# Kernel tuning notes

Hardware: AMD Instinct MI355X
Metric: run time of the kernel (lower is better)

## Reference

```python
import jax, jax.numpy as jnp
import numpy as np

HEADS = 8
DIM_HEAD = 64
SCALE = 10.0
EPS = 1e-12  # F.normalize eps


def setup_inputs() -> dict:
    key = jax.random.key(0)
    k1, k2, k3, k4 = jax.random.split(key, 4)
    dim, hidden = 256, HEADS * DIM_HEAD
    x = jax.random.normal(k1, (8, dim, 32, 32), dtype=jnp.float32)
    w_qkv = jax.random.normal(k2, (3 * hidden, dim), dtype=jnp.float32) * (1.0 / np.sqrt(dim))
    w_out = jax.random.normal(k3, (dim, hidden), dtype=jnp.float32) * (1.0 / np.sqrt(hidden))
    b_out = jax.random.normal(k4, (dim,), dtype=jnp.float32) * 0.01
    return {"x": x, "w_qkv": w_qkv, "w_out": w_out, "b_out": b_out}


def _l2norm_last(t):
    # matches F.normalize(t, dim=-1): t / max(||t||_2, eps)
    n = jnp.sqrt(jnp.sum(t * t, axis=-1, keepdims=True))
    return t / jnp.maximum(n, EPS)


def reference(x, w_qkv, w_out, b_out):
    b, c, hh, ww = x.shape
    n = hh * ww
    # 1x1 conv == channel matmul
    qkv = jnp.einsum('bcxy,oc->boxy', x, w_qkv)  # (b, 3*hidden, h, w)
    q, k, v = jnp.split(qkv, 3, axis=1)
    # 'b (h c) x y -> b h c (x y)'
    to_heads = lambda t: t.reshape(b, HEADS, DIM_HEAD, n)
    q, k, v = to_heads(q), to_heads(k), to_heads(v)
    # NOTE: l2norm over the LAST axis = spatial token axis n (faithful to source)
    q = _l2norm_last(q)
    k = _l2norm_last(k)
    sim = jnp.einsum('bhdi,bhdj->bhij', q, k) * SCALE  # (b, h, n, n)
    attn = jax.nn.softmax(sim, axis=-1)
    out = jnp.einsum('bhij,bhdj->bhid', attn, v)  # (b, h, n, d)
    # 'b h (x y) d -> b (h d) x y'
    out = out.transpose(0, 1, 3, 2).reshape(b, HEADS * DIM_HEAD, hh, ww)
    return jnp.einsum('bcxy,oc->boxy', out, w_out) + b_out[None, :, None, None]
```

## Files before the change

### kernel.cpp

```cpp
#include <hip/hip_runtime.h>
#include <math.h>

#define NHEADS 8
#define DHEAD  64
#define HIDDEN 512
#define CIN    256
#define NTOK   1024
#define QK_SCALE 10.0f
#define LOG2E 1.44269504088896f
#define MSHIFT 10.5f
#define MBIAS  (-MSHIFT * LOG2E)
#define NSPLIT 4

typedef __bf16 bf16x8 __attribute__((ext_vector_type(8)));
typedef float  f32x4  __attribute__((ext_vector_type(4)));
typedef unsigned u32x4 __attribute__((ext_vector_type(4)));
typedef unsigned short u16x8 __attribute__((ext_vector_type(8)));
typedef unsigned short u16x4 __attribute__((ext_vector_type(4)));

__device__ inline unsigned short f2bf(float f) {
    unsigned u = __builtin_bit_cast(unsigned, f);
    u = (u + 0x7FFFu + ((u >> 16) & 1u)) >> 16;
    return (unsigned short)u;
}

__device__ inline unsigned pk2(float a, float b) {
    return (unsigned)f2bf(a) | ((unsigned)f2bf(b) << 16);
}

__device__ inline unsigned pk2t(float a, float b) {
    return (__builtin_bit_cast(unsigned, a) >> 16) |
           (__builtin_bit_cast(unsigned, b) & 0xFFFF0000u);
}
__device__ inline float trunc_bf(float f) {
    return __builtin_bit_cast(float, __builtin_bit_cast(unsigned, f) & 0xFFFF0000u);
}

__device__ inline float bf2f(unsigned short u) {
    return __builtin_bit_cast(float, (unsigned)u << 16);
}

__device__ inline bf16x8 cvt8(const float* p) {
    float4 a = *(const float4*)p;
    float4 b = *(const float4*)(p + 4);
    u16x8 t;
    t[0] = f2bf(a.x); t[1] = f2bf(a.y); t[2] = f2bf(a.z); t[3] = f2bf(a.w);
    t[4] = f2bf(b.x); t[5] = f2bf(b.y); t[6] = f2bf(b.z); t[7] = f2bf(b.w);
    return __builtin_bit_cast(bf16x8, t);
}

__global__ __launch_bounds__(256)
void cvt_x_kernel(const float* __restrict__ x, unsigned short* __restrict__ xt) {
    const int b  = blockIdx.z;
    const int c0 = blockIdx.y * 64;
    const int n0 = blockIdx.x * 64;
    const float* src = x + ((size_t)b * CIN + c0) * NTOK + n0;
    unsigned short* dst = xt + ((size_t)b * NTOK + n0) * CIN + c0;

    __shared__ float T[64][65];
    const int t = threadIdx.x;
    {
        const int nq = t & 15, cg = t >> 4;
        #pragma unroll
        for (int rr = 0; rr < 4; ++rr) {
            const int c = cg + rr * 16;
            float4 v = *(const float4*)(src + (size_t)c * NTOK + nq * 4);
            T[c][nq * 4 + 0] = v.x;
            T[c][nq * 4 + 1] = v.y;
            T[c][nq * 4 + 2] = v.z;
            T[c][nq * 4 + 3] = v.w;
        }
    }
    __syncthreads();
    {
        const int n = t >> 2, cq = t & 3;
        alignas(16) unsigned short tmp[16];
        #pragma unroll
        for (int e = 0; e < 16; ++e)
            tmp[e] = f2bf(T[cq * 16 + e][n]);
        *(uint4*)(dst + (size_t)n * CIN + cq * 16)     = *(uint4*)&tmp[0];
        *(uint4*)(dst + (size_t)n * CIN + cq * 16 + 8) = *(uint4*)&tmp[8];
    }
}

__global__ __launch_bounds__(256)
void cvt_w_kernel(const float* __restrict__ wq, const float* __restrict__ wo,
                  unsigned short* __restrict__ wqb, unsigned short* __restrict__ wob) {
    const size_t i = ((size_t)blockIdx.x * 256 + threadIdx.x) * 8;
    if (i < (size_t)1536 * 256) {
        *(bf16x8*)(wqb + i) = cvt8(wq + i);
    } else {
        const size_t j = i - (size_t)1536 * 256;
        *(bf16x8*)(wob + j) = cvt8(wo + j);
    }
}

__global__ __launch_bounds__(256)
void gemm1_kernel(const unsigned short* __restrict__ wqb,
                  const unsigned short* __restrict__ xt,
                  float* __restrict__ qt,
                  unsigned short* __restrict__ vb,
                  float* __restrict__ ss) {
    const int b  = blockIdx.z;
    const int bm = blockIdx.y * 128;
    const int bn = blockIdx.x * 128;
    const int wave = threadIdx.x >> 6, lane = threadIdx.x & 63;
    const int lo = lane & 15, hi = lane >> 4;
    const int wm = bm + (wave >> 1) * 64;
    const int wn = bn + (wave & 1) * 64;

    const unsigned short* Ab = wqb + (size_t)(wm + lo) * CIN + hi * 8;
    const unsigned short* Bb = xt + ((size_t)b * NTOK + wn + lo) * CIN + hi * 8;

    f32x4 acc[4][4];
    #pragma unroll
    for (int mi = 0; mi < 4; ++mi)
        #pragma unroll
        for (int ni = 0; ni < 4; ++ni) acc[mi][ni] = (f32x4){0.f, 0.f, 0.f, 0.f};

    for (int k0 = 0; k0 < CIN; k0 += 32) {
        bf16x8 a[4], bf[4];
        #pragma unroll
        for (int mi = 0; mi < 4; ++mi) a[mi]  = *(const bf16x8*)(Ab + (size_t)mi * 16 * CIN + k0);
        #pragma unroll
        for (int ni = 0; ni < 4; ++ni) bf[ni] = *(const bf16x8*)(Bb + (size_t)ni * 16 * CIN + k0);
        #pragma unroll
        for (int mi = 0; mi < 4; ++mi)
            #pragma unroll
            for (int ni = 0; ni < 4; ++ni)
                acc[mi][ni] = __builtin_amdgcn_mfma_f32_16x16x32_bf16(a[mi], bf[ni], acc[mi][ni], 0, 0, 0);
    }

    __shared__ unsigned short VL[4][32][72];

    if (bm < 1024) {
        const int isK = (wm >= 512) ? 1 : 0;
        const int ch0 = wm & 511;
        const int head = ch0 >> 6;
        float* dst = qt + (((size_t)isK * 64 + b * 8 + head) * NTOK) * DHEAD;
        #pragma unroll
        for (int mi = 0; mi < 4; ++mi) {
            const int d = mi * 16 + hi * 4;
            #pragma unroll
            for (int ni = 0; ni < 4; ++ni) {
                const int n = wn + ni * 16 + lo;
                *(f32x4*)(dst + (size_t)n * DHEAD + d) = acc[mi][ni];
            }
        }
        float p[4][4];
        #pragma unroll
        for (int mi = 0; mi < 4; ++mi)
            #pragma unroll
            for (int r = 0; r < 4; ++r) {
                float s = 0.f;
                #pragma unroll
                for (int ni = 0; ni < 4; ++ni) s += acc[mi][ni][r] * acc[mi][ni][r];
                p[mi][r] = s;
            }
        #pragma unroll
        for (int off = 1; off < 16; off <<= 1)
            #pragma unroll
            for (int mi = 0; mi < 4; ++mi)
                #pragma unroll
                for (int r = 0; r < 4; ++r)
                    p[mi][r] += __shfl_xor(p[mi][r], off, 64);
        if (lo == 0) {
            #pragma unroll
            for (int mi = 0; mi < 4; ++mi)
                #pragma unroll
                for (int r = 0; r < 4; ++r)
                    atomicAdd(&ss[(size_t)b * 1024 + isK * 512 + ch0 + mi * 16 + hi * 4 + r], p[mi][r]);
        }
    } else {
        const int ch0 = wm - 1024;
        #pragma unroll
        for (int half = 0; half < 2; ++half) {
            #pragma unroll
            for (int mm = 0; mm < 2; ++mm) {
                const int mi = half * 2 + mm;
                #pragma unroll
                for (int ni = 0; ni < 4; ++ni)
                    #pragma unroll
                    for (int r = 0; r < 4; ++r)
                        VL[wave][mm * 16 + hi * 4 + r][ni * 16 + lo] = f2bf(acc[mi][ni][r]);
            }
            #pragma unroll
            for (int i = 0; i < 4; ++i) {
                const int flat = i * 64 + lane;
                const int row = flat >> 3, c = flat & 7;
                const int tb = c >> 2, hg = c & 3;
                const uint2 vlo = *(uint2*)&VL[wave][row][tb * 32 + hg * 4];
                const uint2 vhi = *(uint2*)&VL[wave][row][tb * 32 + hg * 4 + 16];
                uint4 v = make_uint4(vlo.x, vlo.y, vhi.x, vhi.y);
                const int ch = ch0 + half * 32 + row;
                *(uint4*)(vb + ((size_t)b * HIDDEN + ch) * NTOK + wn + c * 8) = v;
            }
        }
    }
}

__global__ __launch_bounds__(256)
void scale_cvt_kernel(const float* __restrict__ qt, const float* __restrict__ ss,
                      unsigned short* __restrict__ qs, unsigned short* __restrict__ ks) {
    const size_t idx = ((size_t)blockIdx.x * 256 + threadIdx.x) * 8;
    const size_t half = (size_t)64 * NTOK * DHEAD;
    const int isK = idx >= half;
    const size_t rem = idx - (size_t)isK * half;
    const int bh = (int)(rem >> 16);
    const int d0 = (int)(rem & 63);
    const int b  = bh >> 3;
    const int ch = isK * 512 + (bh & 7) * 64 + d0;
    const float scl = isK ? 1.0f : QK_SCALE;

    const float* ip = qt + idx;
    float4 v0 = *(const float4*)ip;
    float4 v1 = *(const float4*)(ip + 4);
    float4 q0 = *(const float4*)(ss + (size_t)b * 1024 + ch);
    float4 q1 = *(const float4*)(ss + (size_t)b * 1024 + ch + 4);
    float4 s0, s1;
    s0.x = 1.0f / fmaxf(sqrtf(q0.x), 1e-12f); s0.y = 1.0f / fmaxf(sqrtf(q0.y), 1e-12f);
    s0.z = 1.0f / fmaxf(sqrtf(q0.z), 1e-12f); s0.w = 1.0f / fmaxf(sqrtf(q0.w), 1e-12f);
    s1.x = 1.0f / fmaxf(sqrtf(q1.x), 1e-12f); s1.y = 1.0f / fmaxf(sqrtf(q1.y), 1e-12f);
    s1.z = 1.0f / fmaxf(sqrtf(q1.z), 1e-12f); s1.w = 1.0f / fmaxf(sqrtf(q1.w), 1e-12f);
    u16x8 t;
    t[0] = f2bf(v0.x * s0.x * scl); t[1] = f2bf(v0.y * s0.y * scl);
    t[2] = f2bf(v0.z * s0.z * scl); t[3] = f2bf(v0.w * s0.w * scl);
    t[4] = f2bf(v1.x * s1.x * scl); t[5] = f2bf(v1.y * s1.y * scl);
    t[6] = f2bf(v1.z * s1.z * scl); t[7] = f2bf(v1.w * s1.w * scl);
    *(u16x8*)((isK ? ks : qs) + rem) = t;
}

__global__ __launch_bounds__(128)
void attn_mfma_kernel(const unsigned short* __restrict__ qs,
                      const unsigned short* __restrict__ ks,
                      const unsigned short* __restrict__ vb,
                      unsigned short* __restrict__ po, float* __restrict__ pml) {
    const int hw = blockIdx.x;
    const int virt = (hw & 7) * 512 + (hw >> 3);
    const int bh  = virt >> 6;
    const int sub = virt & 63;
    const int it  = sub & 15;
    const int js  = sub >> 4;
    const int b = bh >> 3, h = bh & 7;

    const int lane = threadIdx.x & 63;
    const int wave = threadIdx.x >> 6;
    const int lo = lane & 15;
    const int hi = lane >> 4;
    const int iw = it * 64 + wave * 32;

    const unsigned short* qbh = qs + (size_t)bh * NTOK * DHEAD;
    const unsigned short* kbh = ks + (size_t)bh * NTOK * DHEAD;
    const unsigned short* vbh = vb + ((size_t)b * HIDDEN + h * DHEAD) * NTOK;

    bf16x8 aQ[2][2];
    #pragma unroll
    for (int f = 0; f < 2; ++f) {
        const unsigned short* qp = qbh + (size_t)(iw + f * 16 + lo) * DHEAD + hi * 8;
        aQ[f][0] = *(const bf16x8*)qp;
        aQ[f][1] = *(const bf16x8*)(qp + 32);
    }

    float lsum4[2][4];
    #pragma unroll
    for (int f = 0; f < 2; ++f)
        #pragma unroll
        for (int r = 0; r < 4; ++r) lsum4[f][r] = 0.0f;
    f32x4 acc[2][4];
    #pragma unroll
    for (int f = 0; f < 2; ++f)
        #pragma unroll
        for (int ds = 0; ds < 4; ++ds) acc[f][ds] = (f32x4){0.f, 0.f, 0.f, 0.f};

    #pragma unroll 2
    for (int jt = 0; jt < 4; ++jt) {
        const int j0 = js * 256 + jt * 64;

        bf16x8 bV[4][2];
        #pragma unroll
        for (int ds = 0; ds < 4; ++ds) {
            const unsigned short* vp = vbh + (size_t)(ds * 16 + lo) * NTOK + j0 + hi * 8;
            bV[ds][0] = *(const bf16x8*)vp;
            bV[ds][1] = *(const bf16x8*)(vp + 32);
        }

        bf16x8 bK[4][2];
        #pragma unroll
        for (int jj = 0; jj < 4; ++jj) {
            const unsigned short* kp = kbh + (size_t)(j0 + jj * 16 + lo) * DHEAD + hi * 8;
            bK[jj][0] = *(const bf16x8*)kp;
            bK[jj][1] = *(const bf16x8*)(kp + 32);
        }

        f32x4 s[2][4];
        __builtin_amdgcn_s_setprio(1);
        #pragma unroll
        for (int jj = 0; jj < 4; ++jj)
            #pragma unroll
            for (int f = 0; f < 2; ++f) {
                f32x4 c = (f32x4){0.f, 0.f, 0.f, 0.f};
                c = __builtin_amdgcn_mfma_f32_16x16x32_bf16(bK[jj][0], aQ[f][0], c, 0, 0, 0);
                c = __builtin_amdgcn_mfma_f32_16x16x32_bf16(bK[jj][1], aQ[f][1], c, 0, 0, 0);
                s[f][jj] = c;
            }
        __builtin_amdgcn_s_setprio(0);

        unsigned pw[2][2][4];
        #pragma unroll
        for (int f = 0; f < 2; ++f) {
            #pragma unroll
            for (int jj = 0; jj < 4; ++jj)
                #pragma unroll
                for (int r = 0; r < 4; ++r) {
                    const float p = __builtin_amdgcn_exp2f(fmaf(s[f][jj][r], LOG2E, MBIAS));
                    s[f][jj][r] = p;
                    lsum4[f][r] += trunc_bf(p);
                }
            #pragma unroll
            for (int t = 0; t < 2; ++t) {
                pw[f][t][0] = pk2t(s[f][2 * t][0],     s[f][2 * t][1]);
                pw[f][t][1] = pk2t(s[f][2 * t][2],     s[f][2 * t][3]);
                pw[f][t][2] = pk2t(s[f][2 * t + 1][0], s[f][2 * t + 1][1]);
                pw[f][t][3] = pk2t(s[f][2 * t + 1][2], s[f][2 * t + 1][3]);
            }
        }

        __builtin_amdgcn_s_setprio(1);
        #pragma unroll
        for (int ds = 0; ds < 4; ++ds)
            #pragma unroll
            for (int f = 0; f < 2; ++f)
                #pragma unroll
                for (int t = 0; t < 2; ++t) {
                    const bf16x8 bp = __builtin_bit_cast(bf16x8,
                        (u32x4){pw[f][t][0], pw[f][t][1], pw[f][t][2], pw[f][t][3]});
                    acc[f][ds] = __builtin_amdgcn_mfma_f32_16x16x32_bf16(bV[ds][t], bp, acc[f][ds], 0, 0, 0);
                }
        __builtin_amdgcn_s_setprio(0);
    }

    float lsum[2];
    #pragma unroll
    for (int f = 0; f < 2; ++f) {
        lsum[f] = (lsum4[f][0] + lsum4[f][1]) + (lsum4[f][2] + lsum4[f][3]);
        lsum[f] += __shfl_xor(lsum[f], 16, 64);
        lsum[f] += __shfl_xor(lsum[f], 32, 64);
    }

    unsigned short* pob = po + ((size_t)(js * 64 + bh) * NTOK + iw) * DHEAD;
    #pragma unroll
    for (int f = 0; f < 2; ++f) {
        #pragma unroll
        for (int ds = 0; ds < 4; ++ds) {
            uint2 w;
            w.x = pk2(acc[f][ds][0], acc[f][ds][1]);
            w.y = pk2(acc[f][ds][2], acc[f][ds][3]);
            *(uint2*)(pob + (size_t)(f * 16 + lo) * DHEAD + ds * 16 + hi * 4) = w;
        }
        if (hi == 0)
            pml[(size_t)(js * 64 + bh) * NTOK + iw + f * 16 + lo] = lsum[f];
    }
}

__global__ __launch_bounds__(256)
void combine_kernel(const unsigned short* __restrict__ po, const float* __restrict__ pml,
                    unsigned short* __restrict__ attn_t) {
    const size_t fl = ((size_t)blockIdx.x * 256 + threadIdx.x) * 8;
    const int bh  = (int)(fl >> 16);
    const int rem = (int)(fl & 65535);
    const int row = rem >> 6;
    const int d   = rem & 63;
    const int b = bh >> 3, h = bh & 7;
    const size_t SS = (size_t)64 * NTOK * DHEAD;

    float l = 0.f;
    #pragma unroll
    for (int s = 0; s < NSPLIT; ++s)
        l += pml[(size_t)(s * 64 + bh) * NTOK + row];
    const float inv = 1.0f / l;

    float o[8] = {};
    #pragma unroll
    for (int s = 0; s < NSPLIT; ++s) {
        const u16x8 v = *(const u16x8*)(po + s * SS + fl);
        #pragma unroll
        for (int e = 0; e < 8; ++e) o[e] += bf2f(v[e]);
    }
    u16x8 r;
    #pragma unroll
    for (int e = 0; e < 8; ++e) r[e] = f2bf(o[e] * inv);
    *(u16x8*)(attn_t + ((size_t)b * NTOK + row) * HIDDEN + h * DHEAD + d) = r;
}

__global__ __launch_bounds__(128)
void gemm2_kernel(const unsigned short* __restrict__ wob,
                  const unsigned short* __restrict__ attn_t,
                  const float* __restrict__ b_out,
                  float* __restrict__ out) {
    const int b  = blockIdx.z;
    const int bm = blockIdx.y * 64;
    const int bn = blockIdx.x * 128;
    const int wave = threadIdx.x >> 6, lane = threadIdx.x & 63;
    const int lo = lane & 15, hi = lane >> 4;
    const int wn = bn + wave * 64;

    const unsigned short* Ab = wob + (size_t)(bm + lo) * HIDDEN + hi * 8;
    const unsigned short* Bb = attn_t + ((size_t)b * NTOK + wn + lo) * HIDDEN + hi * 8;

    f32x4 acc[4][4];
    #pragma unroll
    for (int mi = 0; mi < 4; ++mi)
        #pragma unroll
        for (int ni = 0; ni < 4; ++ni) acc[mi][ni] = (f32x4){0.f, 0.f, 0.f, 0.f};

    for (int k0 = 0; k0 < HIDDEN; k0 += 32) {
        bf16x8 a[4], bf[4];
        #pragma unroll
        for (int mi = 0; mi < 4; ++mi) a[mi]  = *(const bf16x8*)(Ab + (size_t)mi * 16 * HIDDEN + k0);
        #pragma unroll
        for (int ni = 0; ni < 4; ++ni) bf[ni] = *(const bf16x8*)(Bb + (size_t)ni * 16 * HIDDEN + k0);
        #pragma unroll
        for (int mi = 0; mi < 4; ++mi)
            #pragma unroll
            for (int ni = 0; ni < 4; ++ni)
                acc[mi][ni] = __builtin_amdgcn_mfma_f32_16x16x32_bf16(a[mi], bf[ni], acc[mi][ni], 0, 0, 0);
    }

    __shared__ float OL[2][32][69];
    #pragma unroll
    for (int half = 0; half < 2; ++half) {
        #pragma unroll
        for (int mm = 0; mm < 2; ++mm) {
            const int mi = half * 2 + mm;
            #pragma unroll
            for (int ni = 0; ni < 4; ++ni)
                #pragma unroll
                for (int r = 0; r < 4; ++r)
                    OL[wave][mm * 16 + hi * 4 + r][ni * 16 + lo] = acc[mi][ni][r];
        }
        #pragma unroll
        for (int i = 0; i < 8; ++i) {
            const int flat = i * 64 + lane;
            const int row = flat >> 4, c = flat & 15;
            float4 v = *(float4*)&OL[wave][row][c * 4];
            const int m = bm + half * 32 + row;
            const float bb = b_out[m];
            v.x += bb; v.y += bb; v.z += bb; v.w += bb;
            *(float4*)(out + ((size_t)b * CIN + m) * NTOK + wn + c * 4) = v;
        }
    }
}

extern "C" void kernel_launch(void* const* d_in, const int* in_sizes, int n_in,
                              void* d_out, int out_size, void* d_ws, size_t ws_size,
                              hipStream_t stream) {
    const float* x     = (const float*)d_in[0];
    const float* w_qkv = (const float*)d_in[1];
    const float* w_out = (const float*)d_in[2];
    const float* b_out = (const float*)d_in[3];
    float* out = (float*)d_out;

    char* ws = (char*)d_ws;
    unsigned short* xt  = (unsigned short*)(ws);
    unsigned short* wqb = (unsigned short*)(ws + 4194304);
    unsigned short* wob = (unsigned short*)(ws + 4980736);
    float*          ss  = (float*)(ws + 5242880);
    unsigned short* qs  = (unsigned short*)(ws + 5308416);
    unsigned short* ks  = (unsigned short*)(ws + 13697024);
    unsigned short* vb  = (unsigned short*)(ws + 22085632);
    float*          qt  = (float*)(ws + 30474240);
    unsigned short* po  = (unsigned short*)(ws + 30474240);
    unsigned short* attn_t = (unsigned short*)(ws + 5308416);
    float*          pml = (float*)(ws + 64028672);

    hipMemsetAsync(ss, 0, 8 * 1024 * sizeof(float), stream);

    cvt_x_kernel<<<dim3(16, 4, 8), 256, 0, stream>>>(x, xt);
    cvt_w_kernel<<<256, 256, 0, stream>>>(w_qkv, w_out, wqb, wob);

    gemm1_kernel<<<dim3(8, 12, 8), 256, 0, stream>>>(wqb, xt, qt, vb, ss);

    scale_cvt_kernel<<<4096, 256, 0, stream>>>(qt, ss, qs, ks);

    attn_mfma_kernel<<<4096, 128, 0, stream>>>(qs, ks, vb, po, pml);

    combine_kernel<<<2048, 256, 0, stream>>>(po, pml, attn_t);

    gemm2_kernel<<<dim3(8, 4, 8), 128, 0, stream>>>(wob, attn_t, b_out, out);
}
```

Baseline: 207.8 us.

## Drop split-K attention and combine kernel; tile V into contiguous 64x64 blocks

Removes the 4-way key split, so each attention block processes all 1024 keys and normalizes its output directly into attn_t, which eliminates the partial-output buffers and the combine kernel launch. V is rewritten by gemm1 into contiguous 64x64 tiles per (b,h,key-tile) so each V load in the attention loop reads a compact block. The trade-off is a grid that drops from 4096 to 1024 blocks of 2 waves, giving less parallelism per CU and longer serial loops in exchange for less global traffic and one fewer launch.

Result: faster. 196.9 us (-5.2%).

```diff
diff --git a/kernel.cpp b/kernel.cpp
--- a/kernel.cpp
+++ b/kernel.cpp
@@ -10,7 +10,6 @@
 #define LOG2E 1.44269504088896f
 #define MSHIFT 10.5f
 #define MBIAS  (-MSHIFT * LOG2E)
-#define NSPLIT 4
 
 typedef __bf16 bf16x8 __attribute__((ext_vector_type(8)));
 typedef float  f32x4  __attribute__((ext_vector_type(4)));
@@ -173,6 +172,8 @@
         }
     } else {
         const int ch0 = wm - 1024;
+        const int h = ch0 >> 6;
+        unsigned short* tile = vb + (((size_t)b * 8 + h) * 16 + (wn >> 6)) * 4096;
         #pragma unroll
         for (int half = 0; half < 2; ++half) {
             #pragma unroll
@@ -192,8 +193,8 @@
                 const uint2 vlo = *(uint2*)&VL[wave][row][tb * 32 + hg * 4];
                 const uint2 vhi = *(uint2*)&VL[wave][row][tb * 32 + hg * 4 + 16];
                 uint4 v = make_uint4(vlo.x, vlo.y, vhi.x, vhi.y);
-                const int ch = ch0 + half * 32 + row;
-                *(uint4*)(vb + ((size_t)b * HIDDEN + ch) * NTOK + wn + c * 8) = v;
+                const int d = half * 32 + row;
+                *(uint4*)(tile + (size_t)d * 64 + c * 8) = v;
             }
         }
     }
@@ -234,13 +235,11 @@
 void attn_mfma_kernel(const unsigned short* __restrict__ qs,
                       const unsigned short* __restrict__ ks,
                       const unsigned short* __restrict__ vb,
-                      unsigned short* __restrict__ po, float* __restrict__ pml) {
+                      unsigned short* __restrict__ attn_t) {
     const int hw = blockIdx.x;
-    const int virt = (hw & 7) * 512 + (hw >> 3);
-    const int bh  = virt >> 6;
-    const int sub = virt & 63;
-    const int it  = sub & 15;
-    const int js  = sub >> 4;
+    const int virt = (hw & 7) * 128 + (hw >> 3);
+    const int bh = virt >> 4;
+    const int it = virt & 15;
     const int b = bh >> 3, h = bh & 7;
 
     const int lane = threadIdx.x & 63;
@@ -251,7 +250,7 @@
 
     const unsigned short* qbh = qs + (size_t)bh * NTOK * DHEAD;
     const unsigned short* kbh = ks + (size_t)bh * NTOK * DHEAD;
-    const unsigned short* vbh = vb + ((size_t)b * HIDDEN + h * DHEAD) * NTOK;
+    const unsigned short* vbh = vb + (size_t)bh * 16 * 4096;
 
     bf16x8 aQ[2][2];
     #pragma unroll
@@ -273,15 +272,18 @@
         for (int ds = 0; ds < 4; ++ds) acc[f][ds] = (f32x4){0.f, 0.f, 0.f, 0.f};
 
     #pragma unroll 2
-    for (int jt = 0; jt < 4; ++jt) {
-        const int j0 = js * 256 + jt * 64;
+    for (int jt = 0; jt < 16; ++jt) {
+        const int j0 = jt * 64;
 
         bf16x8 bV[4][2];
-        #pragma unroll
-        for (int ds = 0; ds < 4; ++ds) {
-            const unsigned short* vp = vbh + (size_t)(ds * 16 + lo) * NTOK + j0 + hi * 8;
-            bV[ds][0] = *(const bf16x8*)vp;
-            bV[ds][1] = *(const bf16x8*)(vp + 32);
+        {
+            const unsigned short* vt = vbh + (size_t)jt * 4096;
+            #pragma unroll
+            for (int ds = 0; ds < 4; ++ds) {
+                const unsigned short* vp = vt + (ds * 16 + lo) * 64 + hi * 8;
+                bV[ds][0] = *(const bf16x8*)vp;
+                bV[ds][1] = *(const bf16x8*)(vp + 32);
+            }
         }
 
         bf16x8 bK[4][2];
@@ -347,49 +349,18 @@
         lsum[f] += __shfl_xor(lsum[f], 32, 64);
     }
 
-    unsigned short* pob = po + ((size_t)(js * 64 + bh) * NTOK + iw) * DHEAD;
+    unsigned short* at = attn_t + ((size_t)b * NTOK + iw) * HIDDEN + h * DHEAD;
     #pragma unroll
     for (int f = 0; f < 2; ++f) {
+        const float inv = 1.0f / lsum[f];
         #pragma unroll
         for (int ds = 0; ds < 4; ++ds) {
             uint2 w;
-            w.x = pk2(acc[f][ds][0], acc[f][ds][1]);
-            w.y = pk2(acc[f][ds][2], acc[f][ds][3]);
-            *(uint2*)(pob + (size_t)(f * 16 + lo) * DHEAD + ds * 16 + hi * 4) = w;
-        }
-        if (hi == 0)
-            pml[(size_t)(js * 64 + bh) * NTOK + iw + f * 16 + lo] = lsum[f];
-    }
-}
-
-__global__ __launch_bounds__(256)
-void combine_kernel(const unsigned short* __restrict__ po, const float* __restrict__ pml,
-                    unsigned short* __restrict__ attn_t) {
-    const size_t fl = ((size_t)blockIdx.x * 256 + threadIdx.x) * 8;
-    const int bh  = (int)(fl >> 16);
-    const int rem = (int)(fl & 65535);
-    const int row = rem >> 6;
-    const int d   = rem & 63;
-    const int b = bh >> 3, h = bh & 7;
-    const size_t SS = (size_t)64 * NTOK * DHEAD;
-
-    float l = 0.f;
-    #pragma unroll
-    for (int s = 0; s < NSPLIT; ++s)
-        l += pml[(size_t)(s * 64 + bh) * NTOK + row];
-    const float inv = 1.0f / l;
-
-    float o[8] = {};
-    #pragma unroll
-    for (int s = 0; s < NSPLIT; ++s) {
-        const u16x8 v = *(const u16x8*)(po + s * SS + fl);
-        #pragma unroll
-        for (int e = 0; e < 8; ++e) o[e] += bf2f(v[e]);
-    }
-    u16x8 r;
-    #pragma unroll
-    for (int e = 0; e < 8; ++e) r[e] = f2bf(o[e] * inv);
-    *(u16x8*)(attn_t + ((size_t)b * NTOK + row) * HIDDEN + h * DHEAD + d) = r;
+            w.x = pk2(acc[f][ds][0] * inv, acc[f][ds][1] * inv);
+            w.y = pk2(acc[f][ds][2] * inv, acc[f][ds][3] * inv);
+            *(uint2*)(at + (size_t)(f * 16 + lo) * HIDDEN + ds * 16 + hi * 4) = w;
+        }
+    }
 }
 
 __global__ __launch_bounds__(128)
@@ -469,9 +440,7 @@
     unsigned short* ks  = (unsigned short*)(ws + 13697024);
     unsigned short* vb  = (unsigned short*)(ws + 22085632);
     float*          qt  = (float*)(ws + 30474240);
-    unsigned short* po  = (unsigned short*)(ws + 30474240);
-    unsigned short* attn_t = (unsigned short*)(ws + 5308416);
-    float*          pml = (float*)(ws + 64028672);
+    unsigned short* attn_t = (unsigned short*)(ws + 30474240);
 
     hipMemsetAsync(ss, 0, 8 * 1024 * sizeof(float), stream);
 
@@ -482,9 +451,7 @@
 
     scale_cvt_kernel<<<4096, 256, 0, stream>>>(qt, ss, qs, ks);
 
-    attn_mfma_kernel<<<4096, 128, 0, stream>>>(qs, ks, vb, po, pml);
-
-    combine_kernel<<<2048, 256, 0, stream>>>(po, pml, attn_t);
+    attn_mfma_kernel<<<1024, 128, 0, stream>>>(qs, ks, vb, attn_t);
 
     gemm2_kernel<<<dim3(8, 4, 8), 128, 0, stream>>>(wob, attn_t, b_out, out);
 }
```
